# Performance work log

Hardware: AMD Instinct MI355X
Metric: run time of the kernel (lower is better)

## Reference

```python
import jax, jax.numpy as jnp
import numpy as np


def sine_encode_2d(pos, d):
    # pos: (..., 2) normalized relative positions in [-1, 1]; output (..., d)
    # standard sinusoidal encoding per coordinate, d/2 dims each (sin/cos pairs)
    d_half = d // 2
    n_freq = d_half // 2
    freqs = jnp.exp(-jnp.log(jnp.float32(10000.0)) * jnp.arange(n_freq, dtype=jnp.float32) / n_freq)
    parts = []
    for i in range(2):
        ang = pos[..., i:i + 1] * freqs  # (..., n_freq)
        parts.append(jnp.sin(ang))
        parts.append(jnp.cos(ang))
    return jnp.concatenate(parts, axis=-1)


def rpe_bias(W_rpe, t_q, f_q, t_k, f_k, N_t, N_f, d_rpe):
    dt_norm = jnp.arange(-(N_t - 1), N_t, dtype=jnp.float32) / max(N_t - 1, 1)
    df_norm = jnp.arange(-(N_f - 1), N_f, dtype=jnp.float32) / max(N_f - 1, 1)
    DT, DF = jnp.meshgrid(dt_norm, df_norm, indexing='ij')       # (2Nt-1, 2Nf-1)
    rel = jnp.stack([DT, DF], axis=-1)                            # (2Nt-1, 2Nf-1, 2)
    enc = sine_encode_2d(rel, d_rpe)                              # (2Nt-1, 2Nf-1, d_rpe)
    table = enc @ W_rpe.T                                         # (2Nt-1, 2Nf-1, h)
    n_df = 2 * N_f - 1
    flat = table.reshape(-1, table.shape[-1])                     # ((2Nt-1)*(2Nf-1), h)
    dt_idx = t_q[:, None] - t_k[None, :] + (N_t - 1)              # (Nq, Nk)
    df_idx = f_q[:, None] - f_k[None, :] + (N_f - 1)
    flat_idx = jnp.clip(dt_idx * n_df + df_idx, 0, flat.shape[0] - 1)
    bias = flat[flat_idx]                                         # (Nq, Nk, h)
    return jnp.transpose(bias, (2, 0, 1))                         # (h, Nq, Nk)


def setup_inputs() -> dict:
    key = jax.random.key(0)
    ks = jax.random.split(key, 12)
    B, N_t, N_f, d_model, n_heads, d_rpe = 8, 14, 72, 256, 8, 32
    N = N_t * N_f
    s = 1.0 / np.sqrt(d_model)
    return {
        'q_tokens': jax.random.normal(ks[0], (B, N, d_model), jnp.float32),
        'k_tokens': jax.random.normal(ks[1], (B, N, d_model), jnp.float32),
        'v_tokens': jax.random.normal(ks[2], (B, N, d_model), jnp.float32),
        't_q': jax.random.randint(ks[3], (N,), 0, N_t),
        'f_q': jax.random.randint(ks[4], (N,), 0, N_f),
        't_k': jax.random.randint(ks[5], (N,), 0, N_t),
        'f_k': jax.random.randint(ks[6], (N,), 0, N_f),
        'N_t': N_t,
        'N_f': N_f,
        'W_q': jax.random.normal(ks[7], (d_model, d_model), jnp.float32) * s,
        'W_k': jax.random.normal(ks[8], (d_model, d_model), jnp.float32) * s,
        'W_v': jax.random.normal(ks[9], (d_model, d_model), jnp.float32) * s,
        'W_o': jax.random.normal(ks[10], (d_model, d_model), jnp.float32) * s,
        'W_rpe': jax.random.normal(ks[11], (n_heads, d_rpe), jnp.float32) * (1.0 / np.sqrt(d_rpe)),
    }


def reference(q_tokens, k_tokens, v_tokens, t_q, f_q, t_k, f_k, N_t, N_f,
              W_q, W_k, W_v, W_o, W_rpe):
    B, N_q, d_model = q_tokens.shape
    N_k = k_tokens.shape[1]
    h = W_rpe.shape[0]
    d_rpe = W_rpe.shape[1]
    dk = d_model // h
    scale = jnp.float32(np.sqrt(dk))
    Q = (q_tokens @ W_q.T).reshape(B, N_q, h, dk)
    K = (k_tokens @ W_k.T).reshape(B, N_k, h, dk)
    V = (v_tokens @ W_v.T).reshape(B, N_k, h, dk)
    scores = jnp.einsum('bqhd,bkhd->bhqk', Q, K) / scale          # (B, h, Nq, Nk)
    bias = rpe_bias(W_rpe, t_q, f_q, t_k, f_k, N_t, N_f, d_rpe)   # (h, Nq, Nk)
    attn = jax.nn.softmax(scores + bias[None], axis=-1)
    out = jnp.einsum('bhqk,bkhd->bqhd', attn, V).reshape(B, N_q, d_model)
    return out @ W_o.T
```

## Files before the change

### kernel.cpp

```cpp
#include <hip/hip_runtime.h>

#define B_    8
#define N_    1008
#define D_    256
#define H_    8
#define DK_   32
#define NT_   14
#define NF_   72
#define RF_   143
#define TAB_  3861
#define NFREQ_ 8
#define BND_  (B_*N_*D_)

typedef _Float16 half8_t __attribute__((ext_vector_type(8)));
typedef _Float16 half4_t __attribute__((ext_vector_type(4)));
typedef float    f32x4   __attribute__((ext_vector_type(4)));

__global__ void cvt_tokens(const float* __restrict__ a, const float* __restrict__ b,
                           const float* __restrict__ c, _Float16* __restrict__ oa,
                           _Float16* __restrict__ ob, _Float16* __restrict__ oc)
{
    const float* src; _Float16* dst;
    if (blockIdx.y == 0)      { src = a; dst = oa; }
    else if (blockIdx.y == 1) { src = b; dst = ob; }
    else                      { src = c; dst = oc; }
    size_t i = ((size_t)blockIdx.x * 256 + threadIdx.x) * 4;
    float4 v = *(const float4*)&src[i];
    half4_t h = { (_Float16)v.x, (_Float16)v.y, (_Float16)v.z, (_Float16)v.w };
    *(half4_t*)&dst[i] = h;
}

__global__ void rpe_table_kernel(const float* __restrict__ W_rpe,
                                 const int* __restrict__ t_q, const int* __restrict__ f_q,
                                 const int* __restrict__ t_k, const int* __restrict__ f_k,
                                 _Float16* __restrict__ table, int* __restrict__ aq,
                                 int* __restrict__ bk)
{
    int idx = blockIdx.x * blockDim.x + threadIdx.x;
    if (idx < N_) {
        aq[idx] = t_q[idx] * RF_ + f_q[idx];
        bk[idx] = (NT_ - 1) * RF_ + (NF_ - 1) - (t_k[idx] * RF_ + f_k[idx]);
    }
    if (idx < TAB_) {
        int it = idx / RF_;
        int jf = idx - it * RF_;
        float dt = (float)(it - (NT_ - 1)) / (float)(NT_ - 1);
        float df = (float)(jf - (NF_ - 1)) / (float)(NF_ - 1);
        float enc[32];
#pragma unroll
        for (int i = 0; i < NFREQ_; i++) {
            float fr = expf(-9.210340371976184f * (float)i / (float)NFREQ_);
            float at = dt * fr, af = df * fr;
            enc[i]            = sinf(at);
            enc[NFREQ_ + i]   = cosf(at);
            enc[2*NFREQ_ + i] = sinf(af);
            enc[3*NFREQ_ + i] = cosf(af);
        }
#pragma unroll
        for (int hh = 0; hh < H_; hh++) {
            float s = 0.f;
#pragma unroll
            for (int j = 0; j < 32; j++) s += enc[j] * W_rpe[hh * 32 + j];
            table[hh * TAB_ + idx] = (_Float16)s;
        }
    }
}

template <int MODE>
__global__ __launch_bounds__(256, 4) void gemm16(const _Float16* __restrict__ A,
                                                 const float* __restrict__ W,
                                                 void* __restrict__ outp, float scale)
{
    __shared__ __align__(16) _Float16 fw[8 * 4 * 64 * 8];
    const int tid = threadIdx.x;
    const int w = tid >> 6, lane = tid & 63, quad = lane >> 4, l15 = lane & 15;
    const int m0 = blockIdx.x * 64, n0 = blockIdx.y * 64;
#pragma unroll
    for (int p = 0; p < 8; p++) {
        int g = p * 256 + tid;
        int ch = g >> 8, rem = g & 255, nt = rem >> 6, L = rem & 63;
        const float* src = &W[(size_t)(n0 + nt * 16 + (L & 15)) * D_ + ch * 32 + ((L >> 4) & 3) * 8];
        float4 w0 = *(const float4*)src;
        float4 w1 = *(const float4*)(src + 4);
        half8_t hv = { (_Float16)w0.x, (_Float16)w0.y, (_Float16)w0.z, (_Float16)w0.w,
                       (_Float16)w1.x, (_Float16)w1.y, (_Float16)w1.z, (_Float16)w1.w };
        *(half8_t*)&fw[g * 8] = hv;
    }
    __syncthreads();

    f32x4 acc[4] = { {0,0,0,0}, {0,0,0,0}, {0,0,0,0}, {0,0,0,0} };
    const _Float16* Arow = &A[(size_t)(m0 + w * 16 + l15) * D_];
#pragma unroll
    for (int ch = 0; ch < 8; ch++) {
        half8_t af = *(const half8_t*)&Arow[ch * 32 + quad * 8];
#pragma unroll
        for (int nt = 0; nt < 4; nt++) {
            half8_t bf = *(const half8_t*)&fw[((ch * 4 + nt) * 64 + lane) * 8];
            acc[nt] = __builtin_amdgcn_mfma_f32_16x16x32_f16(af, bf, acc[nt], 0, 0, 0);
        }
    }
    const int mbase = m0 + w * 16 + quad * 4;
    if (MODE == 0) {
        _Float16* out = (_Float16*)outp;
#pragma unroll
        for (int nt = 0; nt < 4; nt++) {
            int n = n0 + nt * 16 + l15;
            int hh = n >> 5, d = n & 31;
#pragma unroll
            for (int r = 0; r < 4; r++) {
                int m = mbase + r, bb = m / N_, q = m - bb * N_;
                out[(((size_t)bb * H_ + hh) * N_ + q) * DK_ + d] = (_Float16)(acc[nt][r] * scale);
            }
        }
    } else if (MODE == 1) {
        _Float16* out = (_Float16*)outp;
        int bb = mbase / N_, q = mbase - bb * N_;
#pragma unroll
        for (int nt = 0; nt < 4; nt++) {
            int n = n0 + nt * 16 + l15;
            int hh = n >> 5, d = n & 31;
            half4_t o = { (_Float16)acc[nt][0], (_Float16)acc[nt][1],
                          (_Float16)acc[nt][2], (_Float16)acc[nt][3] };
            *(half4_t*)&out[(((size_t)bb * H_ + hh) * DK_ + d) * N_ + q] = o;
        }
    } else {
        float* out = (float*)outp;
#pragma unroll
        for (int nt = 0; nt < 4; nt++) {
            int n = n0 + nt * 16 + l15;
#pragma unroll
            for (int r = 0; r < 4; r++) {
                out[(size_t)(mbase + r) * D_ + n] = acc[nt][r];
            }
        }
    }
}

__global__ __launch_bounds__(256, 4) void attn16(const _Float16* __restrict__ Qh,
    const _Float16* __restrict__ Kh, const _Float16* __restrict__ Vt,
    const _Float16* __restrict__ tabh, const int* __restrict__ aq,
    const int* __restrict__ bk, _Float16* __restrict__ AO)
{
    __shared__ __align__(16) _Float16 tab_s[TAB_ + 3];
    __shared__ __align__(16) int      bk_s[N_];
    __shared__ __align__(16) _Float16 fk[2][2048];
    __shared__ __align__(16) _Float16 fv[2][2048];
    __shared__ __align__(16) _Float16 plds[4][16][72];

    const int tid = threadIdx.x;
    const int w = tid >> 6, lane = tid & 63, quad = lane >> 4, l15 = lane & 15;
    const int bh = blockIdx.y;
    const int q0 = blockIdx.x * 64;
    const int b = bh >> 3, hh = bh & 7;

    const _Float16* Kb = Kh + (size_t)bh * N_ * DK_;
    const _Float16* Vb = Vt + (size_t)bh * DK_ * N_;
    const _Float16* th = tabh + (size_t)hh * TAB_;
    for (int i = tid; i < TAB_; i += 256) tab_s[i] = th[i];
    for (int i = tid; i < N_; i += 256)  bk_s[i] = bk[i];

    const int qg = q0 + w * 16 + l15;
    const int qc = qg < N_ ? qg : N_ - 1;
    half8_t qf = *(const half8_t*)&Qh[((size_t)bh * N_ + qc) * DK_ + quad * 8];
    const int aql = aq[qc];

    float m_run = -1e30f, l_run = 0.f;
    f32x4 O[2] = { {0,0,0,0}, {0,0,0,0} };

    {
        int krow = ((tid >> 6) & 3) * 16 + (tid & 15);
        *(half8_t*)&fk[0][tid * 8] = *(const half8_t*)&Kb[(size_t)krow * DK_ + ((tid >> 4) & 3) * 8];
        int vrow = ((tid >> 6) & 1) * 16 + (tid & 15);
        int vcol = (tid >> 7) * 32 + ((tid >> 4) & 3) * 8;
        *(half8_t*)&fv[0][tid * 8] = *(const half8_t*)&Vb[(size_t)vrow * N_ + vcol];
    }
    __syncthreads();

    for (int kt = 0; kt < 16; kt++) {
        const int cb = kt & 1;
        const int k0 = kt * 64;
        if (kt < 15) {
            int nk0 = k0 + 64;
            int krow = nk0 + ((tid >> 6) & 3) * 16 + (tid & 15);
            if (krow > N_ - 1) krow = N_ - 1;
            *(half8_t*)&fk[cb ^ 1][tid * 8] =
                *(const half8_t*)&Kb[(size_t)krow * DK_ + ((tid >> 4) & 3) * 8];
            int vrow = ((tid >> 6) & 1) * 16 + (tid & 15);
            int vcol = nk0 + (tid >> 7) * 32 + ((tid >> 4) & 3) * 8;
            if (vcol > N_ - 8) vcol = N_ - 8;
            *(half8_t*)&fv[cb ^ 1][tid * 8] =
                *(const half8_t*)&Vb[(size_t)vrow * N_ + vcol];
        }
        f32x4 S[4];
#pragma unroll
        for (int mt = 0; mt < 4; mt++) {
            half8_t kf = *(const half8_t*)&fk[cb][(mt * 64 + lane) * 8];
            f32x4 z = {0.f, 0.f, 0.f, 0.f};
            S[mt] = __builtin_amdgcn_mfma_f32_16x16x32_f16(kf, qf, z, 0, 0, 0);
        }
        float tmax = -1e30f;
#pragma unroll
        for (int mt = 0; mt < 4; mt++) {
#pragma unroll
            for (int r = 0; r < 4; r++) {
                int kg = k0 + mt * 16 + quad * 4 + r;
                float s;
                if (kg < N_) s = S[mt][r] + (float)tab_s[aql + bk_s[kg]];
                else         s = -1e30f;
                S[mt][r] = s;
                tmax = fmaxf(tmax, s);
            }
        }
        tmax = fmaxf(tmax, __shfl_xor(tmax, 16, 64));
        tmax = fmaxf(tmax, __shfl_xor(tmax, 32, 64));
        float mnew = fmaxf(m_run, tmax);
        float alpha = __expf(m_run - mnew);
        m_run = mnew;
        float tsum = 0.f;
#pragma unroll
        for (int mt = 0; mt < 4; mt++) {
            float p0 = __expf(S[mt][0] - mnew);
            float p1 = __expf(S[mt][1] - mnew);
            float p2 = __expf(S[mt][2] - mnew);
            float p3 = __expf(S[mt][3] - mnew);
            tsum += (p0 + p1) + (p2 + p3);
            half4_t ph = { (_Float16)p0, (_Float16)p1, (_Float16)p2, (_Float16)p3 };
            *(half4_t*)&plds[w][l15][mt * 16 + quad * 4] = ph;
        }
        tsum += __shfl_xor(tsum, 16, 64);
        tsum += __shfl_xor(tsum, 32, 64);
        l_run = l_run * alpha + tsum;
        O[0] = O[0] * alpha;
        O[1] = O[1] * alpha;
#pragma unroll
        for (int mt2 = 0; mt2 < 2; mt2++) {
#pragma unroll
            for (int c = 0; c < 2; c++) {
                half8_t pf = *(const half8_t*)&plds[w][l15][c * 32 + quad * 8];
                half8_t vf = *(const half8_t*)&fv[cb][((c * 2 + mt2) * 64 + lane) * 8];
                O[mt2] = __builtin_amdgcn_mfma_f32_16x16x32_f16(vf, pf, O[mt2], 0, 0, 0);
            }
        }
        __syncthreads();
    }

    if (qg < N_) {
        float inv = 1.f / l_run;
#pragma unroll
        for (int mt2 = 0; mt2 < 2; mt2++) {
            half4_t o = { (_Float16)(O[mt2][0] * inv), (_Float16)(O[mt2][1] * inv),
                          (_Float16)(O[mt2][2] * inv), (_Float16)(O[mt2][3] * inv) };
            *(half4_t*)&AO[((size_t)b * N_ + qg) * D_ + hh * DK_ + mt2 * 16 + quad * 4] = o;
        }
    }
}

extern "C" void kernel_launch(void* const* d_in, const int* in_sizes, int n_in,
                              void* d_out, int out_size, void* d_ws, size_t ws_size,
                              hipStream_t stream)
{
    const float* q_tokens = (const float*)d_in[0];
    const float* k_tokens = (const float*)d_in[1];
    const float* v_tokens = (const float*)d_in[2];
    const int*   t_q      = (const int*)d_in[3];
    const int*   f_q      = (const int*)d_in[4];
    const int*   t_k      = (const int*)d_in[5];
    const int*   f_k      = (const int*)d_in[6];
    const float* W_q   = (const float*)d_in[9];
    const float* W_k   = (const float*)d_in[10];
    const float* W_v   = (const float*)d_in[11];
    const float* W_o   = (const float*)d_in[12];
    const float* W_rpe = (const float*)d_in[13];

    _Float16* ws   = (_Float16*)d_ws;
    _Float16* Qtok = ws;
    _Float16* Ktok = Qtok + BND_;
    _Float16* Vtok = Ktok + BND_;
    _Float16* Qhp  = Vtok + BND_;
    _Float16* Khp  = Qhp + BND_;
    _Float16* Vth  = Khp + BND_;
    _Float16* AO   = Vth + BND_;
    _Float16* tabh = AO + BND_;
    int* aq = (int*)(tabh + 30896);
    int* bk = aq + 1024;

    cvt_tokens<<<dim3(2016, 3), 256, 0, stream>>>(q_tokens, k_tokens, v_tokens,
                                                  Qtok, Ktok, Vtok);
    rpe_table_kernel<<<dim3(16), dim3(256), 0, stream>>>(W_rpe, t_q, f_q, t_k, f_k,
                                                         tabh, aq, bk);
    const float qscale = 0.17677669529663687f;
    gemm16<0><<<dim3(126, 4), dim3(256), 0, stream>>>(Qtok, W_q, Qhp, qscale);
    gemm16<0><<<dim3(126, 4), dim3(256), 0, stream>>>(Ktok, W_k, Khp, 1.0f);
    gemm16<1><<<dim3(126, 4), dim3(256), 0, stream>>>(Vtok, W_v, Vth, 1.0f);

    attn16<<<dim3(16, 64), dim3(256), 0, stream>>>(Qhp, Khp, Vth, tabh, aq, bk, AO);

    gemm16<2><<<dim3(126, 4), dim3(256), 0, stream>>>(AO, W_o, d_out, 1.0f);
}
```

Measured before the change: 175.5 us.

## Fold RPE bias into augmented QK dot product and fuse projection kernels

The relative-position bias is rewritten as a dot product using sin/cos angle-difference identities. Each query row gains 32 extra head dims built from its own positions and W_rpe, and each key row gains 32 extra dims of cos/sin of its positions, so the bias comes out of the QK MFMA. This removes the per-score LDS table gather. The fp32 token conversion is fused into a single QKV GEMM launch with 128x128 tiles, the attention kernel processes 128 queries per block, and the output GEMM uses larger tiles. In exchange the QK inner dimension doubles, and the bias is now computed in fp16 from sin/cos products, which may lose precision.

```diff
diff --git a/kernel.cpp b/kernel.cpp
--- a/kernel.cpp
+++ b/kernel.cpp
@@ -5,252 +5,314 @@
 #define D_    256
 #define H_    8
 #define DK_   32
-#define NT_   14
-#define NF_   72
-#define RF_   143
-#define TAB_  3861
-#define NFREQ_ 8
+#define DA_   64
 #define BND_  (B_*N_*D_)
 
 typedef _Float16 half8_t __attribute__((ext_vector_type(8)));
 typedef _Float16 half4_t __attribute__((ext_vector_type(4)));
 typedef float    f32x4   __attribute__((ext_vector_type(4)));
 
-__global__ void cvt_tokens(const float* __restrict__ a, const float* __restrict__ b,
-                           const float* __restrict__ c, _Float16* __restrict__ oa,
-                           _Float16* __restrict__ ob, _Float16* __restrict__ oc)
-{
-    const float* src; _Float16* dst;
-    if (blockIdx.y == 0)      { src = a; dst = oa; }
-    else if (blockIdx.y == 1) { src = b; dst = ob; }
-    else                      { src = c; dst = oc; }
-    size_t i = ((size_t)blockIdx.x * 256 + threadIdx.x) * 4;
-    float4 v = *(const float4*)&src[i];
-    half4_t h = { (_Float16)v.x, (_Float16)v.y, (_Float16)v.z, (_Float16)v.w };
-    *(half4_t*)&dst[i] = h;
-}
-
-__global__ void rpe_table_kernel(const float* __restrict__ W_rpe,
-                                 const int* __restrict__ t_q, const int* __restrict__ f_q,
-                                 const int* __restrict__ t_k, const int* __restrict__ f_k,
-                                 _Float16* __restrict__ table, int* __restrict__ aq,
-                                 int* __restrict__ bk)
-{
-    int idx = blockIdx.x * blockDim.x + threadIdx.x;
-    if (idx < N_) {
-        aq[idx] = t_q[idx] * RF_ + f_q[idx];
-        bk[idx] = (NT_ - 1) * RF_ + (NF_ - 1) - (t_k[idx] * RF_ + f_k[idx]);
-    }
-    if (idx < TAB_) {
-        int it = idx / RF_;
-        int jf = idx - it * RF_;
-        float dt = (float)(it - (NT_ - 1)) / (float)(NT_ - 1);
-        float df = (float)(jf - (NF_ - 1)) / (float)(NF_ - 1);
-        float enc[32];
-#pragma unroll
-        for (int i = 0; i < NFREQ_; i++) {
-            float fr = expf(-9.210340371976184f * (float)i / (float)NFREQ_);
-            float at = dt * fr, af = df * fr;
-            enc[i]            = sinf(at);
-            enc[NFREQ_ + i]   = cosf(at);
-            enc[2*NFREQ_ + i] = sinf(af);
-            enc[3*NFREQ_ + i] = cosf(af);
-        }
-#pragma unroll
-        for (int hh = 0; hh < H_; hh++) {
-            float s = 0.f;
-#pragma unroll
-            for (int j = 0; j < 32; j++) s += enc[j] * W_rpe[hh * 32 + j];
-            table[hh * TAB_ + idx] = (_Float16)s;
-        }
-    }
-}
-
-template <int MODE>
-__global__ __launch_bounds__(256, 4) void gemm16(const _Float16* __restrict__ A,
-                                                 const float* __restrict__ W,
-                                                 void* __restrict__ outp, float scale)
-{
-    __shared__ __align__(16) _Float16 fw[8 * 4 * 64 * 8];
+__global__ void prep_kernel(const int* __restrict__ t_q, const int* __restrict__ f_q,
+                            const int* __restrict__ t_k, const int* __restrict__ f_k,
+                            const float* __restrict__ W_rpe,
+                            _Float16* __restrict__ Qa, _Float16* __restrict__ Ka)
+{
+    const float FR[8] = {1.f, 0.31622776601683794f, 0.1f, 0.03162277660168379f,
+                         0.01f, 0.0031622776601683794f, 0.001f, 0.00031622776601683794f};
+    int id = blockIdx.x * 256 + threadIdx.x;
+    if (id < N_ * H_) {
+        int q = id >> 3, h = id & 7;
+        float tq = (float)t_q[q] * (1.f / 13.f);
+        float fq = (float)f_q[q] * (1.f / 71.f);
+        const float* Wh = W_rpe + h * 32;
+        half8_t u0, u1, u2, u3;
+#pragma unroll
+        for (int i = 0; i < 8; i++) {
+            float sa = sinf(tq * FR[i]), ca = cosf(tq * FR[i]);
+            float sb = sinf(fq * FR[i]), cb = cosf(fq * FR[i]);
+            u0[i] = (_Float16)(Wh[i] * sa + Wh[8 + i] * ca);
+            u1[i] = (_Float16)(Wh[8 + i] * sa - Wh[i] * ca);
+            u2[i] = (_Float16)(Wh[16 + i] * sb + Wh[24 + i] * cb);
+            u3[i] = (_Float16)(Wh[24 + i] * sb - Wh[16 + i] * cb);
+        }
+#pragma unroll
+        for (int b = 0; b < 8; b++) {
+            _Float16* dst = &Qa[(((size_t)(b * 8 + h)) * N_ + q) * DA_ + 32];
+            *(half8_t*)(dst + 0) = u0;  *(half8_t*)(dst + 8) = u1;
+            *(half8_t*)(dst + 16) = u2; *(half8_t*)(dst + 24) = u3;
+        }
+    } else if (id < N_ * H_ + N_ * 64) {
+        int id2 = id - N_ * H_;
+        int k = id2 >> 6, bh = id2 & 63;
+        float tk = (float)t_k[k] * (1.f / 13.f);
+        float fk = (float)f_k[k] * (1.f / 71.f);
+        half8_t v0, v1, v2, v3;
+#pragma unroll
+        for (int i = 0; i < 8; i++) {
+            v0[i] = (_Float16)cosf(tk * FR[i]);
+            v1[i] = (_Float16)sinf(tk * FR[i]);
+            v2[i] = (_Float16)cosf(fk * FR[i]);
+            v3[i] = (_Float16)sinf(fk * FR[i]);
+        }
+        _Float16* dst = &Ka[(((size_t)bh) * N_ + k) * DA_ + 32];
+        *(half8_t*)(dst + 0) = v0;  *(half8_t*)(dst + 8) = v1;
+        *(half8_t*)(dst + 16) = v2; *(half8_t*)(dst + 24) = v3;
+    }
+}
+
+__global__ __launch_bounds__(256, 2) void qkv_gemm(
+    const float* __restrict__ q_tok, const float* __restrict__ k_tok,
+    const float* __restrict__ v_tok, const float* __restrict__ Wq,
+    const float* __restrict__ Wk, const float* __restrict__ Wv,
+    _Float16* __restrict__ Qa, _Float16* __restrict__ Ka, _Float16* __restrict__ Vt)
+{
+    __shared__ __align__(16) _Float16 fw[8 * 8 * 64 * 8];
     const int tid = threadIdx.x;
-    const int w = tid >> 6, lane = tid & 63, quad = lane >> 4, l15 = lane & 15;
-    const int m0 = blockIdx.x * 64, n0 = blockIdx.y * 64;
-#pragma unroll
-    for (int p = 0; p < 8; p++) {
+    const int lane = tid & 63, w = tid >> 6, quad = lane >> 4, l15 = lane & 15;
+    const int z = blockIdx.z;
+    const int m0 = blockIdx.x * 128, n0 = blockIdx.y * 128;
+    const float* A = (z == 0) ? q_tok : (z == 1) ? k_tok : v_tok;
+    const float* W = (z == 0) ? Wq : (z == 1) ? Wk : Wv;
+
+#pragma unroll
+    for (int p = 0; p < 16; p++) {
         int g = p * 256 + tid;
-        int ch = g >> 8, rem = g & 255, nt = rem >> 6, L = rem & 63;
+        int ch = g >> 9, rem = g & 511, nt = rem >> 6, L = rem & 63;
         const float* src = &W[(size_t)(n0 + nt * 16 + (L & 15)) * D_ + ch * 32 + ((L >> 4) & 3) * 8];
         float4 w0 = *(const float4*)src;
         float4 w1 = *(const float4*)(src + 4);
-        half8_t hv = { (_Float16)w0.x, (_Float16)w0.y, (_Float16)w0.z, (_Float16)w0.w,
-                       (_Float16)w1.x, (_Float16)w1.y, (_Float16)w1.z, (_Float16)w1.w };
+        half8_t hv = {(_Float16)w0.x, (_Float16)w0.y, (_Float16)w0.z, (_Float16)w0.w,
+                      (_Float16)w1.x, (_Float16)w1.y, (_Float16)w1.z, (_Float16)w1.w};
         *(half8_t*)&fw[g * 8] = hv;
     }
     __syncthreads();
 
-    f32x4 acc[4] = { {0,0,0,0}, {0,0,0,0}, {0,0,0,0}, {0,0,0,0} };
-    const _Float16* Arow = &A[(size_t)(m0 + w * 16 + l15) * D_];
+    f32x4 acc[2][8] = {};
+    const float* Ar0 = &A[(size_t)(m0 + w * 16 + l15) * D_];
+    const float* Ar1 = Ar0 + (size_t)64 * D_;
 #pragma unroll
     for (int ch = 0; ch < 8; ch++) {
-        half8_t af = *(const half8_t*)&Arow[ch * 32 + quad * 8];
-#pragma unroll
-        for (int nt = 0; nt < 4; nt++) {
-            half8_t bf = *(const half8_t*)&fw[((ch * 4 + nt) * 64 + lane) * 8];
-            acc[nt] = __builtin_amdgcn_mfma_f32_16x16x32_f16(af, bf, acc[nt], 0, 0, 0);
-        }
-    }
-    const int mbase = m0 + w * 16 + quad * 4;
-    if (MODE == 0) {
-        _Float16* out = (_Float16*)outp;
-#pragma unroll
-        for (int nt = 0; nt < 4; nt++) {
-            int n = n0 + nt * 16 + l15;
-            int hh = n >> 5, d = n & 31;
-#pragma unroll
-            for (int r = 0; r < 4; r++) {
-                int m = mbase + r, bb = m / N_, q = m - bb * N_;
-                out[(((size_t)bb * H_ + hh) * N_ + q) * DK_ + d] = (_Float16)(acc[nt][r] * scale);
-            }
-        }
-    } else if (MODE == 1) {
-        _Float16* out = (_Float16*)outp;
-        int bb = mbase / N_, q = mbase - bb * N_;
-#pragma unroll
-        for (int nt = 0; nt < 4; nt++) {
-            int n = n0 + nt * 16 + l15;
-            int hh = n >> 5, d = n & 31;
-            half4_t o = { (_Float16)acc[nt][0], (_Float16)acc[nt][1],
-                          (_Float16)acc[nt][2], (_Float16)acc[nt][3] };
-            *(half4_t*)&out[(((size_t)bb * H_ + hh) * DK_ + d) * N_ + q] = o;
-        }
-    } else {
-        float* out = (float*)outp;
-#pragma unroll
-        for (int nt = 0; nt < 4; nt++) {
-            int n = n0 + nt * 16 + l15;
-#pragma unroll
-            for (int r = 0; r < 4; r++) {
-                out[(size_t)(mbase + r) * D_ + n] = acc[nt][r];
-            }
-        }
-    }
-}
-
-__global__ __launch_bounds__(256, 4) void attn16(const _Float16* __restrict__ Qh,
-    const _Float16* __restrict__ Kh, const _Float16* __restrict__ Vt,
-    const _Float16* __restrict__ tabh, const int* __restrict__ aq,
-    const int* __restrict__ bk, _Float16* __restrict__ AO)
-{
-    __shared__ __align__(16) _Float16 tab_s[TAB_ + 3];
-    __shared__ __align__(16) int      bk_s[N_];
-    __shared__ __align__(16) _Float16 fk[2][2048];
+        float4 a00 = *(const float4*)&Ar0[ch * 32 + quad * 8];
+        float4 a01 = *(const float4*)&Ar0[ch * 32 + quad * 8 + 4];
+        float4 a10 = *(const float4*)&Ar1[ch * 32 + quad * 8];
+        float4 a11 = *(const float4*)&Ar1[ch * 32 + quad * 8 + 4];
+        half8_t af0 = {(_Float16)a00.x, (_Float16)a00.y, (_Float16)a00.z, (_Float16)a00.w,
+                       (_Float16)a01.x, (_Float16)a01.y, (_Float16)a01.z, (_Float16)a01.w};
+        half8_t af1 = {(_Float16)a10.x, (_Float16)a10.y, (_Float16)a10.z, (_Float16)a10.w,
+                       (_Float16)a11.x, (_Float16)a11.y, (_Float16)a11.z, (_Float16)a11.w};
+#pragma unroll
+        for (int nt = 0; nt < 8; nt++) {
+            half8_t bf = *(const half8_t*)&fw[((ch * 8 + nt) * 64 + lane) * 8];
+            acc[0][nt] = __builtin_amdgcn_mfma_f32_16x16x32_f16(af0, bf, acc[0][nt], 0, 0, 0);
+            acc[1][nt] = __builtin_amdgcn_mfma_f32_16x16x32_f16(af1, bf, acc[1][nt], 0, 0, 0);
+        }
+    }
+    const float scale = (z == 0) ? 0.17677669529663687f : 1.0f;
+#pragma unroll
+    for (int mt = 0; mt < 2; mt++) {
+        int mbase = m0 + mt * 64 + w * 16 + quad * 4;
+        int b = mbase / N_;
+        int q = mbase - b * N_;
+        if (z < 2) {
+            _Float16* out = (z == 0) ? Qa : Ka;
+#pragma unroll
+            for (int nt = 0; nt < 8; nt++) {
+                int n = n0 + nt * 16 + l15;
+                int hh = n >> 5, d = n & 31;
+                _Float16* dst = &out[(((size_t)(b * 8 + hh)) * N_ + q) * DA_ + d];
+#pragma unroll
+                for (int r = 0; r < 4; r++)
+                    dst[(size_t)r * DA_] = (_Float16)(acc[mt][nt][r] * scale);
+            }
+        } else {
+#pragma unroll
+            for (int nt = 0; nt < 8; nt++) {
+                int n = n0 + nt * 16 + l15;
+                int hh = n >> 5, d = n & 31;
+                half4_t o = {(_Float16)acc[mt][nt][0], (_Float16)acc[mt][nt][1],
+                             (_Float16)acc[mt][nt][2], (_Float16)acc[mt][nt][3]};
+                *(half4_t*)&Vt[(((size_t)(b * 8 + hh)) * DK_ + d) * N_ + q] = o;
+            }
+        }
+    }
+}
+
+__global__ __launch_bounds__(256, 2) void attn(const _Float16* __restrict__ Qa,
+    const _Float16* __restrict__ Ka, const _Float16* __restrict__ Vt,
+    _Float16* __restrict__ AO)
+{
+    __shared__ __align__(16) _Float16 fk[2][4096];
     __shared__ __align__(16) _Float16 fv[2][2048];
-    __shared__ __align__(16) _Float16 plds[4][16][72];
+    __shared__ __align__(16) _Float16 plds[4][2][16][72];
 
     const int tid = threadIdx.x;
-    const int w = tid >> 6, lane = tid & 63, quad = lane >> 4, l15 = lane & 15;
-    const int bh = blockIdx.y;
-    const int q0 = blockIdx.x * 64;
+    const int lane = tid & 63, w = tid >> 6, quad = lane >> 4, l15 = lane & 15;
+    const int bh = blockIdx.y, q0 = blockIdx.x * 128;
     const int b = bh >> 3, hh = bh & 7;
-
-    const _Float16* Kb = Kh + (size_t)bh * N_ * DK_;
+    const _Float16* Kb = Ka + (size_t)bh * N_ * DA_;
     const _Float16* Vb = Vt + (size_t)bh * DK_ * N_;
-    const _Float16* th = tabh + (size_t)hh * TAB_;
-    for (int i = tid; i < TAB_; i += 256) tab_s[i] = th[i];
-    for (int i = tid; i < N_; i += 256)  bk_s[i] = bk[i];
-
-    const int qg = q0 + w * 16 + l15;
-    const int qc = qg < N_ ? qg : N_ - 1;
-    half8_t qf = *(const half8_t*)&Qh[((size_t)bh * N_ + qc) * DK_ + quad * 8];
-    const int aql = aq[qc];
-
-    float m_run = -1e30f, l_run = 0.f;
-    f32x4 O[2] = { {0,0,0,0}, {0,0,0,0} };
+
+    const int s_l15 = tid & 15, s_quad = (tid >> 4) & 3;
+    const int s_mt = tid >> 6;
+    const int s_c = tid >> 7;
+    const int s_mt2 = (tid >> 6) & 1;
+
+    half8_t qf[2][2];
+    int qg[2];
+#pragma unroll
+    for (int g = 0; g < 2; g++) {
+        qg[g] = q0 + w * 32 + g * 16 + l15;
+        int qc = qg[g] < N_ ? qg[g] : N_ - 1;
+        const _Float16* Qrow = &Qa[((size_t)bh * N_ + qc) * DA_];
+        qf[g][0] = *(const half8_t*)&Qrow[quad * 8];
+        qf[g][1] = *(const half8_t*)&Qrow[32 + quad * 8];
+    }
+
+    float m_run[2] = {-1e30f, -1e30f}, l_run[2] = {0.f, 0.f};
+    f32x4 O[2][2] = {};
 
     {
-        int krow = ((tid >> 6) & 3) * 16 + (tid & 15);
-        *(half8_t*)&fk[0][tid * 8] = *(const half8_t*)&Kb[(size_t)krow * DK_ + ((tid >> 4) & 3) * 8];
-        int vrow = ((tid >> 6) & 1) * 16 + (tid & 15);
-        int vcol = (tid >> 7) * 32 + ((tid >> 4) & 3) * 8;
+        int krow = s_mt * 16 + s_l15;
+        *(half8_t*)&fk[0][((s_mt * 2 + 0) * 64 + lane) * 8] =
+            *(const half8_t*)&Kb[(size_t)krow * DA_ + s_quad * 8];
+        *(half8_t*)&fk[0][((s_mt * 2 + 1) * 64 + lane) * 8] =
+            *(const half8_t*)&Kb[(size_t)krow * DA_ + 32 + s_quad * 8];
+        int vrow = s_mt2 * 16 + s_l15;
+        int vcol = s_c * 32 + s_quad * 8;
         *(half8_t*)&fv[0][tid * 8] = *(const half8_t*)&Vb[(size_t)vrow * N_ + vcol];
     }
     __syncthreads();
 
     for (int kt = 0; kt < 16; kt++) {
         const int cb = kt & 1;
-        const int k0 = kt * 64;
         if (kt < 15) {
-            int nk0 = k0 + 64;
-            int krow = nk0 + ((tid >> 6) & 3) * 16 + (tid & 15);
+            int k0n = (kt + 1) * 64;
+            int krow = k0n + s_mt * 16 + s_l15;
             if (krow > N_ - 1) krow = N_ - 1;
-            *(half8_t*)&fk[cb ^ 1][tid * 8] =
-                *(const half8_t*)&Kb[(size_t)krow * DK_ + ((tid >> 4) & 3) * 8];
-            int vrow = ((tid >> 6) & 1) * 16 + (tid & 15);
-            int vcol = nk0 + (tid >> 7) * 32 + ((tid >> 4) & 3) * 8;
+            *(half8_t*)&fk[cb ^ 1][((s_mt * 2 + 0) * 64 + lane) * 8] =
+                *(const half8_t*)&Kb[(size_t)krow * DA_ + s_quad * 8];
+            *(half8_t*)&fk[cb ^ 1][((s_mt * 2 + 1) * 64 + lane) * 8] =
+                *(const half8_t*)&Kb[(size_t)krow * DA_ + 32 + s_quad * 8];
+            int vrow = s_mt2 * 16 + s_l15;
+            int vcol = k0n + s_c * 32 + s_quad * 8;
             if (vcol > N_ - 8) vcol = N_ - 8;
-            *(half8_t*)&fv[cb ^ 1][tid * 8] =
-                *(const half8_t*)&Vb[(size_t)vrow * N_ + vcol];
-        }
-        f32x4 S[4];
+            *(half8_t*)&fv[cb ^ 1][tid * 8] = *(const half8_t*)&Vb[(size_t)vrow * N_ + vcol];
+        }
+        half8_t kf[4][2], vf[4];
 #pragma unroll
         for (int mt = 0; mt < 4; mt++) {
-            half8_t kf = *(const half8_t*)&fk[cb][(mt * 64 + lane) * 8];
-            f32x4 z = {0.f, 0.f, 0.f, 0.f};
-            S[mt] = __builtin_amdgcn_mfma_f32_16x16x32_f16(kf, qf, z, 0, 0, 0);
-        }
-        float tmax = -1e30f;
-#pragma unroll
-        for (int mt = 0; mt < 4; mt++) {
-#pragma unroll
-            for (int r = 0; r < 4; r++) {
-                int kg = k0 + mt * 16 + quad * 4 + r;
-                float s;
-                if (kg < N_) s = S[mt][r] + (float)tab_s[aql + bk_s[kg]];
-                else         s = -1e30f;
-                S[mt][r] = s;
-                tmax = fmaxf(tmax, s);
-            }
-        }
-        tmax = fmaxf(tmax, __shfl_xor(tmax, 16, 64));
-        tmax = fmaxf(tmax, __shfl_xor(tmax, 32, 64));
-        float mnew = fmaxf(m_run, tmax);
-        float alpha = __expf(m_run - mnew);
-        m_run = mnew;
-        float tsum = 0.f;
-#pragma unroll
-        for (int mt = 0; mt < 4; mt++) {
-            float p0 = __expf(S[mt][0] - mnew);
-            float p1 = __expf(S[mt][1] - mnew);
-            float p2 = __expf(S[mt][2] - mnew);
-            float p3 = __expf(S[mt][3] - mnew);
-            tsum += (p0 + p1) + (p2 + p3);
-            half4_t ph = { (_Float16)p0, (_Float16)p1, (_Float16)p2, (_Float16)p3 };
-            *(half4_t*)&plds[w][l15][mt * 16 + quad * 4] = ph;
-        }
-        tsum += __shfl_xor(tsum, 16, 64);
-        tsum += __shfl_xor(tsum, 32, 64);
-        l_run = l_run * alpha + tsum;
-        O[0] = O[0] * alpha;
-        O[1] = O[1] * alpha;
-#pragma unroll
-        for (int mt2 = 0; mt2 < 2; mt2++) {
+            kf[mt][0] = *(const half8_t*)&fk[cb][((mt * 2 + 0) * 64 + lane) * 8];
+            kf[mt][1] = *(const half8_t*)&fk[cb][((mt * 2 + 1) * 64 + lane) * 8];
+        }
+#pragma unroll
+        for (int f2 = 0; f2 < 4; f2++)
+            vf[f2] = *(const half8_t*)&fv[cb][(f2 * 64 + lane) * 8];
+
+#pragma unroll
+        for (int g = 0; g < 2; g++) {
+            f32x4 S[4];
+#pragma unroll
+            for (int mt = 0; mt < 4; mt++) {
+                f32x4 zz = {0.f, 0.f, 0.f, 0.f};
+                zz = __builtin_amdgcn_mfma_f32_16x16x32_f16(kf[mt][0], qf[g][0], zz, 0, 0, 0);
+                S[mt] = __builtin_amdgcn_mfma_f32_16x16x32_f16(kf[mt][1], qf[g][1], zz, 0, 0, 0);
+            }
+            if (kt == 15)
+                S[3] = (f32x4){-1e30f, -1e30f, -1e30f, -1e30f};
+            float tmax = -1e30f;
+#pragma unroll
+            for (int mt = 0; mt < 4; mt++)
+#pragma unroll
+                for (int r = 0; r < 4; r++) tmax = fmaxf(tmax, S[mt][r]);
+            tmax = fmaxf(tmax, __shfl_xor(tmax, 16, 64));
+            tmax = fmaxf(tmax, __shfl_xor(tmax, 32, 64));
+            float mnew = fmaxf(m_run[g], tmax);
+            float alpha = __expf(m_run[g] - mnew);
+            m_run[g] = mnew;
+            float tsum = 0.f;
+#pragma unroll
+            for (int mt = 0; mt < 4; mt++) {
+                float p0 = __expf(S[mt][0] - mnew), p1 = __expf(S[mt][1] - mnew);
+                float p2 = __expf(S[mt][2] - mnew), p3 = __expf(S[mt][3] - mnew);
+                tsum += (p0 + p1) + (p2 + p3);
+                half4_t ph = {(_Float16)p0, (_Float16)p1, (_Float16)p2, (_Float16)p3};
+                *(half4_t*)&plds[w][g][l15][mt * 16 + quad * 4] = ph;
+            }
+            tsum += __shfl_xor(tsum, 16, 64);
+            tsum += __shfl_xor(tsum, 32, 64);
+            l_run[g] = l_run[g] * alpha + tsum;
+            O[g][0] = O[g][0] * alpha;
+            O[g][1] = O[g][1] * alpha;
+        }
+#pragma unroll
+        for (int g = 0; g < 2; g++) {
 #pragma unroll
             for (int c = 0; c < 2; c++) {
-                half8_t pf = *(const half8_t*)&plds[w][l15][c * 32 + quad * 8];
-                half8_t vf = *(const half8_t*)&fv[cb][((c * 2 + mt2) * 64 + lane) * 8];
-                O[mt2] = __builtin_amdgcn_mfma_f32_16x16x32_f16(vf, pf, O[mt2], 0, 0, 0);
+                half8_t pf = *(const half8_t*)&plds[w][g][l15][c * 32 + quad * 8];
+                O[g][0] = __builtin_amdgcn_mfma_f32_16x16x32_f16(vf[c * 2 + 0], pf, O[g][0], 0, 0, 0);
+                O[g][1] = __builtin_amdgcn_mfma_f32_16x16x32_f16(vf[c * 2 + 1], pf, O[g][1], 0, 0, 0);
             }
         }
         __syncthreads();
     }
-
-    if (qg < N_) {
-        float inv = 1.f / l_run;
-#pragma unroll
-        for (int mt2 = 0; mt2 < 2; mt2++) {
-            half4_t o = { (_Float16)(O[mt2][0] * inv), (_Float16)(O[mt2][1] * inv),
-                          (_Float16)(O[mt2][2] * inv), (_Float16)(O[mt2][3] * inv) };
-            *(half4_t*)&AO[((size_t)b * N_ + qg) * D_ + hh * DK_ + mt2 * 16 + quad * 4] = o;
+#pragma unroll
+    for (int g = 0; g < 2; g++) {
+        if (qg[g] < N_) {
+            float inv = 1.f / l_run[g];
+#pragma unroll
+            for (int mt2 = 0; mt2 < 2; mt2++) {
+                half4_t o = {(_Float16)(O[g][mt2][0] * inv), (_Float16)(O[g][mt2][1] * inv),
+                             (_Float16)(O[g][mt2][2] * inv), (_Float16)(O[g][mt2][3] * inv)};
+                *(half4_t*)&AO[((size_t)b * N_ + qg[g]) * D_ + hh * DK_ + mt2 * 16 + quad * 4] = o;
+            }
+        }
+    }
+}
+
+__global__ __launch_bounds__(256, 2) void out_gemm(const _Float16* __restrict__ A,
+    const float* __restrict__ W, float* __restrict__ out)
+{
+    __shared__ __align__(16) _Float16 fw[8 * 8 * 64 * 8];
+    const int tid = threadIdx.x;
+    const int lane = tid & 63, w = tid >> 6, quad = lane >> 4, l15 = lane & 15;
+    const int m0 = blockIdx.x * 128, n0 = blockIdx.y * 128;
+
+#pragma unroll
+    for (int p = 0; p < 16; p++) {
+        int g = p * 256 + tid;
+        int ch = g >> 9, rem = g & 511, nt = rem >> 6, L = rem & 63;
+        const float* src = &W[(size_t)(n0 + nt * 16 + (L & 15)) * D_ + ch * 32 + ((L >> 4) & 3) * 8];
+        float4 w0 = *(const float4*)src;
+        float4 w1 = *(const float4*)(src + 4);
+        half8_t hv = {(_Float16)w0.x, (_Float16)w0.y, (_Float16)w0.z, (_Float16)w0.w,
+                      (_Float16)w1.x, (_Float16)w1.y, (_Float16)w1.z, (_Float16)w1.w};
+        *(half8_t*)&fw[g * 8] = hv;
+    }
+    __syncthreads();
+
+    f32x4 acc[2][8] = {};
+    const _Float16* Ar0 = &A[(size_t)(m0 + w * 16 + l15) * D_];
+    const _Float16* Ar1 = Ar0 + (size_t)64 * D_;
+#pragma unroll
+    for (int ch = 0; ch < 8; ch++) {
+        half8_t af0 = *(const half8_t*)&Ar0[ch * 32 + quad * 8];
+        half8_t af1 = *(const half8_t*)&Ar1[ch * 32 + quad * 8];
+#pragma unroll
+        for (int nt = 0; nt < 8; nt++) {
+            half8_t bf = *(const half8_t*)&fw[((ch * 8 + nt) * 64 + lane) * 8];
+            acc[0][nt] = __builtin_amdgcn_mfma_f32_16x16x32_f16(af0, bf, acc[0][nt], 0, 0, 0);
+            acc[1][nt] = __builtin_amdgcn_mfma_f32_16x16x32_f16(af1, bf, acc[1][nt], 0, 0, 0);
+        }
+    }
+#pragma unroll
+    for (int mt = 0; mt < 2; mt++) {
+        int mbase = m0 + mt * 64 + w * 16 + quad * 4;
+#pragma unroll
+        for (int nt = 0; nt < 8; nt++) {
+            int n = n0 + nt * 16 + l15;
+#pragma unroll
+            for (int r = 0; r < 4; r++)
+                out[(size_t)(mbase + r) * D_ + n] = acc[mt][nt][r];
         }
     }
 }
@@ -272,28 +334,15 @@
     const float* W_o   = (const float*)d_in[12];
     const float* W_rpe = (const float*)d_in[13];
 
-    _Float16* ws   = (_Float16*)d_ws;
-    _Float16* Qtok = ws;
-    _Float16* Ktok = Qtok + BND_;
-    _Float16* Vtok = Ktok + BND_;
-    _Float16* Qhp  = Vtok + BND_;
-    _Float16* Khp  = Qhp + BND_;
-    _Float16* Vth  = Khp + BND_;
-    _Float16* AO   = Vth + BND_;
-    _Float16* tabh = AO + BND_;
-    int* aq = (int*)(tabh + 30896);
-    int* bk = aq + 1024;
-
-    cvt_tokens<<<dim3(2016, 3), 256, 0, stream>>>(q_tokens, k_tokens, v_tokens,
-                                                  Qtok, Ktok, Vtok);
-    rpe_table_kernel<<<dim3(16), dim3(256), 0, stream>>>(W_rpe, t_q, f_q, t_k, f_k,
-                                                         tabh, aq, bk);
-    const float qscale = 0.17677669529663687f;
-    gemm16<0><<<dim3(126, 4), dim3(256), 0, stream>>>(Qtok, W_q, Qhp, qscale);
-    gemm16<0><<<dim3(126, 4), dim3(256), 0, stream>>>(Ktok, W_k, Khp, 1.0f);
-    gemm16<1><<<dim3(126, 4), dim3(256), 0, stream>>>(Vtok, W_v, Vth, 1.0f);
-
-    attn16<<<dim3(16, 64), dim3(256), 0, stream>>>(Qhp, Khp, Vth, tabh, aq, bk, AO);
-
-    gemm16<2><<<dim3(126, 4), dim3(256), 0, stream>>>(AO, W_o, d_out, 1.0f);
-}
+    _Float16* ws = (_Float16*)d_ws;
+    _Float16* Qa = ws;
+    _Float16* Ka = Qa + (size_t)64 * N_ * DA_;
+    _Float16* Vt = Ka + (size_t)64 * N_ * DA_;
+    _Float16* AO = Vt + (size_t)64 * DK_ * N_;
+
+    prep_kernel<<<dim3(284), 256, 0, stream>>>(t_q, f_q, t_k, f_k, W_rpe, Qa, Ka);
+    qkv_gemm<<<dim3(63, 2, 3), 256, 0, stream>>>(q_tokens, k_tokens, v_tokens,
+                                                 W_q, W_k, W_v, Qa, Ka, Vt);
+    attn<<<dim3(8, 64), 256, 0, stream>>>(Qa, Ka, Vt, AO);
+    out_gemm<<<dim3(63, 2), 256, 0, stream>>>(AO, W_o, (float*)d_out);
+}
```

New measurement: 169.5 us. 3.4% less time.
